# Kernel optimization log

Hardware: AMD Instinct MI355X
Metric: run time of the kernel (lower is better)

The kernel has to match this reference:

```python
import jax, jax.numpy as jnp
import numpy as np

COST_CLASS = 1.0
COST_OBJECTNESS = 5.0
COST_GIOU = 2.0
COST_CENTER = 10.0

B, Q, G, C = 32, 1024, 64, 256


def _lsa(cost):
    """Exact rectangular linear sum assignment (Jonker-Volgenant shortest
    augmenting path, same algorithm as scipy.optimize.linear_sum_assignment).
    cost: (R, Cc) float64 numpy array. Returns (row_ind, col_ind), row_ind sorted."""
    transposed = cost.shape[0] > cost.shape[1]
    if transposed:
        cost = cost.T
    n, m = cost.shape
    u = np.zeros(n)
    v = np.zeros(m)
    col4row = np.full(n, -1, dtype=np.int64)
    row4col = np.full(m, -1, dtype=np.int64)
    for cur_row in range(n):
        shortest = np.full(m, np.inf)
        path = np.full(m, -1, dtype=np.int64)
        SC = np.zeros(m, dtype=bool)
        SR_rows = []
        min_val = 0.0
        i = cur_row
        sink = -1
        while sink == -1:
            SR_rows.append(i)
            idx = np.where(~SC)[0]
            r = min_val + cost[i, idx] - u[i] - v[idx]
            better = r < shortest[idx]
            upd = idx[better]
            shortest[upd] = r[better]
            path[upd] = i
            j = idx[np.argmin(shortest[idx])]
            min_val = shortest[j]
            SC[j] = True
            if row4col[j] == -1:
                sink = j
            else:
                i = row4col[j]
        # dual variable update
        u[cur_row] += min_val
        for irow in SR_rows:
            if irow != cur_row:
                u[irow] += min_val - shortest[col4row[irow]]
        v[SC] -= min_val - shortest[SC]
        # augment along the alternating path back to cur_row
        j = sink
        while True:
            i = path[j]
            row4col[j] = i
            col4row[i], j = j, col4row[i]
            if i == cur_row:
                break
    if transposed:
        order = np.argsort(col4row)
        return col4row[order], np.arange(n)[order]
    return np.arange(n), col4row


def setup_inputs() -> dict:
    key = jax.random.key(0)
    k1, k2, k3, k4, k5 = jax.random.split(key, 5)
    return {
        "sem_cls_prob": jax.random.uniform(k1, (B, Q, C), dtype=jnp.float32),
        "objectness_prob": jax.random.uniform(k2, (B, Q), dtype=jnp.float32),
        "center_dist": jax.random.uniform(k3, (B, Q, G), dtype=jnp.float32),
        "gious": jax.random.uniform(k4, (B, Q, G), dtype=jnp.float32),
        "nactual_gt": jax.random.randint(k5, (B,), 0, G, dtype=jnp.int64)
        if jax.config.jax_enable_x64 else jax.random.randint(k5, (B,), 0, G).astype(jnp.int32),
    }


def reference(sem_cls_prob, objectness_prob, center_dist, gious, nactual_gt):
    batchsize, nprop = objectness_prob.shape
    # class_mat == 0 in the original module
    final_cost = (COST_OBJECTNESS * (-objectness_prob[..., None])
                  + COST_CENTER * center_dist
                  + COST_GIOU * (-gious))  # [B, Q, G]
    cost_np = np.asarray(final_cost, dtype=np.float64)
    ngt = np.asarray(nactual_gt)
    per_prop_gt_inds = np.zeros((batchsize, nprop), dtype=np.int64)
    proposal_matched_mask = np.zeros((batchsize, nprop), dtype=np.float32)
    for b in range(batchsize):  # per-batch independent Hungarian (as in source)
        g = int(ngt[b])
        if g > 0:
            rows, cols = _lsa(cost_np[b, :, :g])
            per_prop_gt_inds[b, rows] = cols
            proposal_matched_mask[b, rows] = 1.0
    return jnp.asarray(per_prop_gt_inds), jnp.asarray(proposal_matched_mask)
```

## Files before the change

kernel.cpp:

```cpp
#include <hip/hip_runtime.h>
#include <math.h>

#define B_ 32
#define Q_ 1024
#define G_ 64
#define K16 16

typedef double v16d __attribute__((ext_vector_type(16)));
typedef float  v16f __attribute__((ext_vector_type(16)));
typedef int    v16i __attribute__((ext_vector_type(16)));

#define REP16(OP) OP(0,0) OP(1,1) OP(2,2) OP(3,3) OP(4,4) OP(5,5) OP(6,6) OP(7,7) \
                  OP(8,8) OP(9,9) OP(10,a) OP(11,b) OP(12,c) OP(13,d) OP(14,e) OP(15,f)
#define REP16A(OP,A) OP(A,0,0) OP(A,1,1) OP(A,2,2) OP(A,3,3) OP(A,4,4) OP(A,5,5) OP(A,6,6) OP(A,7,7) \
                     OP(A,8,8) OP(A,9,9) OP(A,10,a) OP(A,11,b) OP(A,12,c) OP(A,13,d) OP(A,14,e) OP(A,15,f)

#define ROR1 0x121
#define ROR2 0x122
#define ROR4 0x124
#define ROR8 0x128
#define BC15 0x142
#define BC31 0x143

template<int CTRL>
__device__ __forceinline__ double dpp_f64(double x) {
    union { double d; int i[2]; } a; a.d = x;
    union { int i[2]; double d; } r;
    r.i[0] = __builtin_amdgcn_update_dpp(a.i[0], a.i[0], CTRL, 0xF, 0xF, false);
    r.i[1] = __builtin_amdgcn_update_dpp(a.i[1], a.i[1], CTRL, 0xF, 0xF, false);
    return r.d;
}
template<int CTRL>
__device__ __forceinline__ int dpp_i32(int x) {
    return __builtin_amdgcn_update_dpp(x, x, CTRL, 0xF, 0xF, false);
}

__device__ __forceinline__ double readlane_f64(double x, int sl) {
    const int s = __builtin_amdgcn_readfirstlane(sl);
    union { double d; int i2[2]; } a; a.d = x;
    union { int i2[2]; double d; } r;
    r.i2[0] = __builtin_amdgcn_readlane(a.i2[0], s);
    r.i2[1] = __builtin_amdgcn_readlane(a.i2[1], s);
    return r.d;
}
__device__ __forceinline__ double readlane_f64c(double x, int sl) {
    union { double d; int i2[2]; } a; a.d = x;
    union { int i2[2]; double d; } r;
    r.i2[0] = __builtin_amdgcn_readlane(a.i2[0], sl);
    r.i2[1] = __builtin_amdgcn_readlane(a.i2[1], sl);
    return r.d;
}
__device__ __forceinline__ float readlane_f32u(float x, int sl) {
    union { float f; int i; } a; a.f = x;
    union { int i; float f; } r;
    r.i = __builtin_amdgcn_readlane(a.i, __builtin_amdgcn_readfirstlane(sl));
    return r.f;
}
__device__ __forceinline__ int readlane_i32(int x, int sl) {
    return __builtin_amdgcn_readlane(x, __builtin_amdgcn_readfirstlane(sl));
}
__device__ __forceinline__ int readlane_i32c(int x, int sl) {
    return __builtin_amdgcn_readlane(x, sl);
}

__device__ __forceinline__ int sel16v_i(v16i p, int s) {
    const int t0_0 = (s & 1) ? p.s1 : p.s0;
    const int t0_1 = (s & 1) ? p.s3 : p.s2;
    const int t0_2 = (s & 1) ? p.s5 : p.s4;
    const int t0_3 = (s & 1) ? p.s7 : p.s6;
    const int t0_4 = (s & 1) ? p.s9 : p.s8;
    const int t0_5 = (s & 1) ? p.sb : p.sa;
    const int t0_6 = (s & 1) ? p.sd : p.sc;
    const int t0_7 = (s & 1) ? p.sf : p.se;
    const int t1_0 = (s & 2) ? t0_1 : t0_0;
    const int t1_1 = (s & 2) ? t0_3 : t0_2;
    const int t1_2 = (s & 2) ? t0_5 : t0_4;
    const int t1_3 = (s & 2) ? t0_7 : t0_6;
    const int a0 = (s & 4) ? t1_1 : t1_0;
    const int a1 = (s & 4) ? t1_3 : t1_2;
    return (s & 8) ? a1 : a0;
}
__device__ __forceinline__ double sel16v_d(v16d p, int s) {
    const double t0_0 = (s & 1) ? p.s1 : p.s0;
    const double t0_1 = (s & 1) ? p.s3 : p.s2;
    const double t0_2 = (s & 1) ? p.s5 : p.s4;
    const double t0_3 = (s & 1) ? p.s7 : p.s6;
    const double t0_4 = (s & 1) ? p.s9 : p.s8;
    const double t0_5 = (s & 1) ? p.sb : p.sa;
    const double t0_6 = (s & 1) ? p.sd : p.sc;
    const double t0_7 = (s & 1) ? p.sf : p.se;
    const double t1_0 = (s & 2) ? t0_1 : t0_0;
    const double t1_1 = (s & 2) ? t0_3 : t0_2;
    const double t1_2 = (s & 2) ? t0_5 : t0_4;
    const double t1_3 = (s & 2) ? t0_7 : t0_6;
    const double a0 = (s & 4) ? t1_1 : t1_0;
    const double a1 = (s & 4) ? t1_3 : t1_2;
    return (s & 8) ? a1 : a0;
}

__device__ __forceinline__ void lexpair(v16d c, int l,
                                        double& gv_o, int& jm_o) {
    const double a0 = fmin(c.s0, c.s1), a1 = fmin(c.s2, c.s3),
                 a2 = fmin(c.s4, c.s5), a3 = fmin(c.s6, c.s7),
                 a4 = fmin(c.s8, c.s9), a5 = fmin(c.sa, c.sb),
                 a6 = fmin(c.sc, c.sd), a7 = fmin(c.se, c.sf);
    const double b0 = fmin(a0, a1), b1 = fmin(a2, a3),
                 b2 = fmin(a4, a5), b3 = fmin(a6, a7);
    const double d0 = fmin(b0, b1), d1 = fmin(b2, b3);
    const double vloc = fmin(d0, d1);
    double v = vloc;
#define VS_(C) { const double pv = dpp_f64<C>(v); v = fmin(pv, v); }
    VS_(ROR1) VS_(ROR2) VS_(ROR4) VS_(ROR8) VS_(BC15) VS_(BC31)
#undef VS_
    const double gv = readlane_f64c(v, 63);
    const int bit3 = (d0 == gv) ? 0 : 1;
    const double bsel = bit3 ? b2 : b0;
    const int bit2 = (bsel == gv) ? 0 : 1;
    const double asel = bit2 ? (bit3 ? a6 : a2) : (bit3 ? a4 : a0);
    const int bit1 = (asel == gv) ? 0 : 1;
    const double csel = bit1 ? (bit2 ? (bit3 ? c.se : c.s6) : (bit3 ? c.sa : c.s2))
                             : (bit2 ? (bit3 ? c.sc : c.s4) : (bit3 ? c.s8 : c.s0));
    const int bit0 = (csel == gv) ? 0 : 1;
    const int kloc = (bit3 << 3) | (bit2 << 2) | (bit1 << 1) | bit0;
    int key = (vloc == gv) ? ((kloc << 6) | l) : 0x7FFFFFFF;
#define KS_(C) { const int pk = dpp_i32<C>(key); key = (pk < key) ? pk : key; }
    KS_(ROR1) KS_(ROR2) KS_(ROR4) KS_(ROR8) KS_(BC15) KS_(BC31)
#undef KS_
    jm_o = readlane_i32c(key, 63);
    gv_o = gv;
}

__global__ __launch_bounds__(256) void build_kernel(
    const float* __restrict__ obj, const float* __restrict__ cd,
    const float* __restrict__ gi, float* __restrict__ ct,
    float* __restrict__ pv, int* __restrict__ pj,
    float* __restrict__ pv2, int* __restrict__ pj2)
{
    __shared__ float tile[64][65];
    const int b  = blockIdx.y;
    const int jb = blockIdx.x << 6;
    const int t  = threadIdx.x;
    const float* objb = obj + (b << 10);
    const float4* cd4 = (const float4*)(cd + ((size_t)b << 16));
    const float4* gi4 = (const float4*)(gi + ((size_t)b << 16));

    #pragma unroll
    for (int p = 0; p < 4; ++p) {
        const int f  = t + (p << 8);
        const int jj = f >> 4;
        const int q  = f & 15;
        const int i0 = q << 2;
        const int j  = jb + jj;
        const float om = __fmul_rn(5.0f, -objb[j]);
        const float4 c4 = cd4[(j << 4) + q];
        const float4 q4 = gi4[(j << 4) + q];
        tile[i0 + 0][jj] = __fadd_rn(__fadd_rn(om, __fmul_rn(10.0f, c4.x)), __fmul_rn(2.0f, -q4.x));
        tile[i0 + 1][jj] = __fadd_rn(__fadd_rn(om, __fmul_rn(10.0f, c4.y)), __fmul_rn(2.0f, -q4.y));
        tile[i0 + 2][jj] = __fadd_rn(__fadd_rn(om, __fmul_rn(10.0f, c4.z)), __fmul_rn(2.0f, -q4.z));
        tile[i0 + 3][jj] = __fadd_rn(__fadd_rn(om, __fmul_rn(10.0f, c4.w)), __fmul_rn(2.0f, -q4.w));
    }
    __syncthreads();
    #pragma unroll
    for (int r = 0; r < 16; ++r) {
        const int idx = (r << 8) + t;
        const int i = idx >> 6, j2 = idx & 63;
        ct[(((size_t)(b << 6) + i) << 10) + jb + j2] = tile[i][j2];
    }
    if (t < 64) {
        float bv = tile[t][0]; int bc = 0;
        float sv = 1e30f;      int sc2 = 0;
        #pragma unroll 8
        for (int c = 1; c < 64; ++c) {
            const float v = tile[t][c];
            const bool t1 = v < bv;
            const bool t2 = (!t1) && (v < sv);
            sv  = t1 ? bv : (t2 ? v : sv);
            sc2 = t1 ? bc : (t2 ? c : sc2);
            bv  = t1 ? v : bv;
            bc  = t1 ? c : bc;
        }
        const int o = (((b << 6) + t) << 4) + blockIdx.x;
        pv[o]  = bv;  pj[o]  = jb + bc;
        pv2[o] = sv;  pj2[o] = jb + sc2;
    }
}

template<class LR>
__device__ __forceinline__ void matcher_core(
    const int l, const int g, LR load_row,
    const float pre_v, const int pre_j, const float sec_v, const int sec_j,
    float* __restrict__ out_ind_b, float* __restrict__ out_mask_b)
{
    const double INF = __builtin_inf();
    double u_rep = 0.0;
    double m_rec = 0.0;
    bool   inSR  = false;
    int    c4r_rep = -1;
    unsigned asg   = 0u;
    unsigned dirty = 0u;
    v16d v_r, sh_r;
    v16i path;
    v16f c_cur, c_i;
#define INI_(K,H) { v_r.s##H = 0.0; sh_r.s##H = 0.0; path.s##H = 0; }
    REP16(INI_)
#undef INI_
#define Z16_(K,H) { c_cur.s##H = 0.0f; c_i.s##H = 0.0f; }
    REP16(Z16_)
#undef Z16_

    for (int cur = 0; cur < g; ++cur) {
        const float pre_vc = readlane_f32u(pre_v, cur);
        int jm = readlane_i32(pre_j, cur);
        double minv = (double)pre_vc;
        bool have_cur = false;
        {
            const int ow1 = jm & 63, sl1 = jm >> 6;
            const unsigned d1 = (unsigned)readlane_i32((int)dirty, ow1);
            if ((d1 >> sl1) & 1u) {
                const float sv_c = readlane_f32u(sec_v, cur);
                const int   sj_c = readlane_i32(sec_j, cur);
                const unsigned d2 = (unsigned)readlane_i32((int)dirty, sj_c & 63);
                if (!((d2 >> (sj_c >> 6)) & 1u) && (sj_c != jm)) {
                    const double vpj = readlane_f64(sel16v_d(v_r, sl1), ow1);
                    const double vA = (double)pre_vc - vpj;
                    const double vB = (double)sv_c;
                    const bool tt = (vB < vA) || ((vB == vA) && (sj_c < jm));
                    minv = tt ? vB : vA;
                    jm   = tt ? sj_c : jm;
                } else {
                    c_cur = load_row(cur); have_cur = true;
                    v16d rr0;
#define RR0_(K,H) rr0.s##H = (double)c_cur.s##H - v_r.s##H;
                    REP16(RR0_)
#undef RR0_
                    lexpair(rr0, l, minv, jm);
                }
            }
        }
        const unsigned long long mk0 = __ballot(c4r_rep == jm);

        if (mk0 == 0ull) {
            u_rep   = (l == cur) ? u_rep + minv : u_rep;
            c4r_rep = (l == cur) ? jm           : c4r_rep;
            asg     = (l == (jm & 63)) ? (asg | (1u << (jm >> 6))) : asg;
        } else {
            if (!have_cur) c_cur = load_row(cur);
            int i = (int)__builtin_ctzll(mk0);
            c_i = load_row(i);
            double ui = readlane_f64(u_rep, i);
            unsigned sc = (l == (jm & 63)) ? (1u << (jm >> 6)) : 0u;
            inSR  = (l == i);
            m_rec = minv;
#define SH0_(K,H) { sh_r.s##H = (double)c_cur.s##H - v_r.s##H; path.s##H = cur; }
            REP16(SH0_)
#undef SH0_

            int sink = -1;
            while (sink < 0) {
                v16d cand;
#define DST_(K,H) { const double rr = ((minv + (double)c_i.s##H) - ui) - v_r.s##H; \
                    const bool notSC = !((sc >> K) & 1u); \
                    const bool upd = notSC && (rr < sh_r.s##H);  \
                    sh_r.s##H = upd ? rr : sh_r.s##H; \
                    path.s##H = upd ? i : path.s##H; \
                    cand.s##H = notSC ? sh_r.s##H : INF; }
                REP16(DST_)
#undef DST_
                lexpair(cand, l, minv, jm);
                const unsigned long long mk = __ballot(c4r_rep == jm);
                if (l == (jm & 63)) sc |= (1u << (jm >> 6));
                if (mk == 0ull) {
                    sink = jm;
                } else {
                    i = (int)__builtin_ctzll(mk);
                    c_i = load_row(i);
                    if (l == i) { inSR = true; m_rec = minv; }
                    ui = readlane_f64(u_rep, i);
                }
            }

            if (l == cur)       u_rep += minv;
            else if (inSR)      u_rep += minv - m_rec;
            unsigned chg = 0u;
#define VUP_(K,H) { const bool in_sc = (sc >> K) & 1u; \
                    const double nv = v_r.s##H - (minv - sh_r.s##H); \
                    chg = (in_sc && (sh_r.s##H != minv)) ? (chg | (1u << K)) : chg; \
                    v_r.s##H = in_sc ? nv : v_r.s##H; }
            REP16(VUP_)
#undef VUP_
            dirty |= chg;

            int j = sink;
            while (true) {
                const int so = j & 63, ss = j >> 6;
                const int ii = readlane_i32(sel16v_i(path, ss), so);
                const int nj = readlane_i32(c4r_rep, ii);
                asg     = (l == so) ? (asg | (1u << ss)) : asg;
                c4r_rep = (l == ii) ? j : c4r_rep;
                j = nj;
                if (ii == cur) break;
            }
        }
    }

#define OUT_(K,H) { const int jj = l + (K << 6); const bool a_ = (asg >> K) & 1u; \
    out_mask_b[jj] = a_ ? 1.0f : 0.0f; \
    if (!a_) out_ind_b[jj] = 0.0f; }
    REP16(OUT_)
#undef OUT_
    if (c4r_rep >= 0) out_ind_b[c4r_rep] = (float)l;
}

__global__ __launch_bounds__(256, 1) void matcher_ws(
    const int* __restrict__ ngt, const float* __restrict__ ct,
    const float* __restrict__ pv, const int* __restrict__ pj,
    const float* __restrict__ pv2, const int* __restrict__ pj2,
    float* __restrict__ out_ind, float* __restrict__ out_mask)
{
    const int b = blockIdx.x;
    const int t = threadIdx.x;
    const float* ctb = ct + ((size_t)(b << 6) << 10);

    if (t >= 64) {
        const float4* c4p = (const float4*)ctb;
        for (int n = t - 64; n < 16384; n += 192) {
            const float4 x = c4p[n];
            asm volatile("" :: "v"(x.x), "v"(x.y), "v"(x.z), "v"(x.w));
        }
        return;
    }

    const int l = t;
    const int g = ngt[b];

    const int base = ((b << 6) + l) << 4;
    const float4* pvq = (const float4*)(pv  + base);
    const int4*   pjq = (const int4*)(pj  + base);
    const float4* svq = (const float4*)(pv2 + base);
    const int4*   sjq = (const int4*)(pj2 + base);
    const float4 pA = pvq[0], pB = pvq[1], pC = pvq[2], pD = pvq[3];
    const int4   jA = pjq[0], jB = pjq[1], jC = pjq[2], jD = pjq[3];
    const float4 sA = svq[0], sB = svq[1], sC = svq[2], sD = svq[3];
    const int4   tA = sjq[0], tB = sjq[1], tC = sjq[2], tD = sjq[3];
    float bv = pA.x; int bj = jA.x; float sv = sA.x; int sj = tA.x;
#define MERGE_(CV,CJ,C2V,C2J) { const bool nb = (CV) < bv; \
    const bool s1 = (C2V) < bv; const bool s2 = (CV) < sv; \
    const float nsv = nb ? (s1 ? (C2V) : bv) : (s2 ? (CV) : sv); \
    const int   nsj = nb ? (s1 ? (C2J) : bj) : (s2 ? (CJ) : sj); \
    bj = nb ? (CJ) : bj; bv = nb ? (CV) : bv; sv = nsv; sj = nsj; }
    MERGE_(pA.y,jA.y,sA.y,tA.y) MERGE_(pA.z,jA.z,sA.z,tA.z) MERGE_(pA.w,jA.w,sA.w,tA.w)
    MERGE_(pB.x,jB.x,sB.x,tB.x) MERGE_(pB.y,jB.y,sB.y,tB.y) MERGE_(pB.z,jB.z,sB.z,tB.z) MERGE_(pB.w,jB.w,sB.w,tB.w)
    MERGE_(pC.x,jC.x,sC.x,tC.x) MERGE_(pC.y,jC.y,sC.y,tC.y) MERGE_(pC.z,jC.z,sC.z,tC.z) MERGE_(pC.w,jC.w,sC.w,tC.w)
    MERGE_(pD.x,jD.x,sD.x,tD.x) MERGE_(pD.y,jD.y,sD.y,tD.y) MERGE_(pD.z,jD.z,sD.z,tD.z) MERGE_(pD.w,jD.w,sD.w,tD.w)
#undef MERGE_

    auto load_row = [&](int ri) -> v16f {
        v16f d; const float* rp_ = ctb + ((size_t)ri << 10) + l;
#define LDW_(D,K,H) D.s##H = rp_[(K) << 6];
        REP16A(LDW_, d)
#undef LDW_
        return d;
    };
    matcher_core(l, g, load_row, bv, bj, sv, sj,
                 out_ind + (b << 10), out_mask + (b << 10));
}

__global__ __launch_bounds__(64, 1) void matcher_nws(
    const float* __restrict__ obj, const float* __restrict__ cd,
    const float* __restrict__ gi, const int* __restrict__ ngt,
    float* __restrict__ out_ind, float* __restrict__ out_mask)
{
    const int b = blockIdx.x;
    const int l = threadIdx.x;
    const int g = ngt[b];
    const float* objb = obj + (b << 10);
    const float* cdb  = cd + ((size_t)b << 16);
    const float* gib  = gi + ((size_t)b << 16);

    v16f objm;
#define OBJI_(K,H) objm.s##H = __fmul_rn(5.0f, -objb[l + (K << 6)]);
    REP16(OBJI_)
#undef OBJI_
    auto load_row = [&](int ri) -> v16f {
        v16f d;
#define LDN_(D,K,H) { const int idx_ = ((l + ((K) << 6)) << 6) + ri; \
    D.s##H = __fadd_rn(__fadd_rn(objm.s##H, __fmul_rn(10.0f, cdb[idx_])), \
                       __fmul_rn(2.0f, -gib[idx_])); }
        REP16A(LDN_, d)
#undef LDN_
        return d;
    };

    float pre_v = 0.0f; int pre_j = 0;
    for (int i = 0; i < g; ++i) {
        v16f c = load_row(i);
        v16d c64;
#define CV_(K,H) c64.s##H = (double)c.s##H;
        REP16(CV_)
#undef CV_
        double gv; int j0;
        lexpair(c64, l, gv, j0);
        pre_v = (l == i) ? (float)gv : pre_v;
        pre_j = (l == i) ? j0 : pre_j;
    }
    matcher_core(l, g, load_row, pre_v, pre_j, pre_v, pre_j,
                 out_ind + (b << 10), out_mask + (b << 10));
}

extern "C" void kernel_launch(void* const* d_in, const int* in_sizes, int n_in,
                              void* d_out, int out_size, void* d_ws, size_t ws_size,
                              hipStream_t stream)
{
    const float* obj = (const float*)d_in[1];
    const float* cd  = (const float*)d_in[2];
    const float* gi  = (const float*)d_in[3];
    const int*   ngt = (const int*)d_in[4];
    float* out0 = (float*)d_out;
    float* out1 = out0 + B_ * Q_;

    const size_t ct_b = (size_t)B_ * G_ * Q_ * sizeof(float);
    const size_t pv_b = (size_t)B_ * G_ * 16 * sizeof(float);
    if (ws_size >= ct_b + 4 * pv_b) {
        float* ct  = (float*)d_ws;
        float* pv  = (float*)((char*)d_ws + ct_b);
        int*   pj  = (int*)  ((char*)d_ws + ct_b + pv_b);
        float* pv2 = (float*)((char*)d_ws + ct_b + 2 * pv_b);
        int*   pj2 = (int*)  ((char*)d_ws + ct_b + 3 * pv_b);
        build_kernel<<<dim3(16, B_), 256, 0, stream>>>(obj, cd, gi, ct, pv, pj, pv2, pj2);
        matcher_ws<<<B_, 256, 0, stream>>>(ngt, ct, pv, pj, pv2, pj2, out0, out1);
    } else {
        matcher_nws<<<B_, 64, 0, stream>>>(obj, cd, gi, ngt, out0, out1);
    }
}
```

Measured before the change: 156.7 us.

## Fuse build and matcher kernels with per-batch flag spin-wait

Merges the cost-build kernel and the matcher kernel into one launch. The first 32 blocks are matchers and the other 512 blocks are builders. Each builder atomically increments a per-batch flag after writing its tile, and each matcher spins until its batch's flag reaches 16. This lets the matcher for one batch start while builds for other batches are still running, and removes the launch boundary between the two kernels. In exchange it adds a memset launch and relies on builder blocks being scheduled while matcher blocks spin. Matchers get the lower block IDs, so they are likely dispatched first, and there is some deadlock risk if builders cannot get resources.

```diff
diff --git a/kernel.cpp b/kernel.cpp
--- a/kernel.cpp
+++ b/kernel.cpp
@@ -130,61 +130,6 @@
     gv_o = gv;
 }
 
-__global__ __launch_bounds__(256) void build_kernel(
-    const float* __restrict__ obj, const float* __restrict__ cd,
-    const float* __restrict__ gi, float* __restrict__ ct,
-    float* __restrict__ pv, int* __restrict__ pj,
-    float* __restrict__ pv2, int* __restrict__ pj2)
-{
-    __shared__ float tile[64][65];
-    const int b  = blockIdx.y;
-    const int jb = blockIdx.x << 6;
-    const int t  = threadIdx.x;
-    const float* objb = obj + (b << 10);
-    const float4* cd4 = (const float4*)(cd + ((size_t)b << 16));
-    const float4* gi4 = (const float4*)(gi + ((size_t)b << 16));
-
-    #pragma unroll
-    for (int p = 0; p < 4; ++p) {
-        const int f  = t + (p << 8);
-        const int jj = f >> 4;
-        const int q  = f & 15;
-        const int i0 = q << 2;
-        const int j  = jb + jj;
-        const float om = __fmul_rn(5.0f, -objb[j]);
-        const float4 c4 = cd4[(j << 4) + q];
-        const float4 q4 = gi4[(j << 4) + q];
-        tile[i0 + 0][jj] = __fadd_rn(__fadd_rn(om, __fmul_rn(10.0f, c4.x)), __fmul_rn(2.0f, -q4.x));
-        tile[i0 + 1][jj] = __fadd_rn(__fadd_rn(om, __fmul_rn(10.0f, c4.y)), __fmul_rn(2.0f, -q4.y));
-        tile[i0 + 2][jj] = __fadd_rn(__fadd_rn(om, __fmul_rn(10.0f, c4.z)), __fmul_rn(2.0f, -q4.z));
-        tile[i0 + 3][jj] = __fadd_rn(__fadd_rn(om, __fmul_rn(10.0f, c4.w)), __fmul_rn(2.0f, -q4.w));
-    }
-    __syncthreads();
-    #pragma unroll
-    for (int r = 0; r < 16; ++r) {
-        const int idx = (r << 8) + t;
-        const int i = idx >> 6, j2 = idx & 63;
-        ct[(((size_t)(b << 6) + i) << 10) + jb + j2] = tile[i][j2];
-    }
-    if (t < 64) {
-        float bv = tile[t][0]; int bc = 0;
-        float sv = 1e30f;      int sc2 = 0;
-        #pragma unroll 8
-        for (int c = 1; c < 64; ++c) {
-            const float v = tile[t][c];
-            const bool t1 = v < bv;
-            const bool t2 = (!t1) && (v < sv);
-            sv  = t1 ? bv : (t2 ? v : sv);
-            sc2 = t1 ? bc : (t2 ? c : sc2);
-            bv  = t1 ? v : bv;
-            bc  = t1 ? c : bc;
-        }
-        const int o = (((b << 6) + t) << 4) + blockIdx.x;
-        pv[o]  = bv;  pj[o]  = jb + bc;
-        pv2[o] = sv;  pj2[o] = jb + sc2;
-    }
-}
-
 template<class LR>
 __device__ __forceinline__ void matcher_core(
     const int l, const int g, LR load_row,
@@ -311,16 +256,83 @@
     if (c4r_rep >= 0) out_ind_b[c4r_rep] = (float)l;
 }
 
-__global__ __launch_bounds__(256, 1) void matcher_ws(
-    const int* __restrict__ ngt, const float* __restrict__ ct,
-    const float* __restrict__ pv, const int* __restrict__ pj,
-    const float* __restrict__ pv2, const int* __restrict__ pj2,
+__global__ __launch_bounds__(256, 4) void fused2_k(
+    const float* __restrict__ obj, const float* __restrict__ cd,
+    const float* __restrict__ gi, const int* __restrict__ ngt,
+    float* __restrict__ ct,
+    float* __restrict__ pv, int* __restrict__ pj,
+    float* __restrict__ pv2, int* __restrict__ pj2,
+    unsigned* __restrict__ flags,
     float* __restrict__ out_ind, float* __restrict__ out_mask)
 {
-    const int b = blockIdx.x;
-    const int t = threadIdx.x;
+    __shared__ float tile[64][65];
+    const int t   = threadIdx.x;
+    const int bid = blockIdx.x;
+
+    if (bid >= B_) {
+        const int n0 = bid - B_;
+        const int b  = (n0 & 7) + (((n0 >> 3) & 3) << 3);
+        const int cb = n0 >> 5;
+        const int jb = cb << 6;
+        const float* objb = obj + (b << 10);
+        const float4* cd4 = (const float4*)(cd + ((size_t)b << 16));
+        const float4* gi4 = (const float4*)(gi + ((size_t)b << 16));
+
+        #pragma unroll
+        for (int p = 0; p < 4; ++p) {
+            const int f  = t + (p << 8);
+            const int jj = f >> 4;
+            const int q  = f & 15;
+            const int i0 = q << 2;
+            const int j  = jb + jj;
+            const float om = __fmul_rn(5.0f, -objb[j]);
+            const float4 c4 = cd4[(j << 4) + q];
+            const float4 q4 = gi4[(j << 4) + q];
+            tile[i0 + 0][jj] = __fadd_rn(__fadd_rn(om, __fmul_rn(10.0f, c4.x)), __fmul_rn(2.0f, -q4.x));
+            tile[i0 + 1][jj] = __fadd_rn(__fadd_rn(om, __fmul_rn(10.0f, c4.y)), __fmul_rn(2.0f, -q4.y));
+            tile[i0 + 2][jj] = __fadd_rn(__fadd_rn(om, __fmul_rn(10.0f, c4.z)), __fmul_rn(2.0f, -q4.z));
+            tile[i0 + 3][jj] = __fadd_rn(__fadd_rn(om, __fmul_rn(10.0f, c4.w)), __fmul_rn(2.0f, -q4.w));
+        }
+        __syncthreads();
+        #pragma unroll
+        for (int r = 0; r < 16; ++r) {
+            const int idx = (r << 8) + t;
+            const int i = idx >> 6, j2 = idx & 63;
+            ct[(((size_t)(b << 6) + i) << 10) + jb + j2] = tile[i][j2];
+        }
+        if (t < 64) {
+            float bv = tile[t][0]; int bc = 0;
+            float sv = 1e30f;      int sc2 = 0;
+            #pragma unroll 8
+            for (int c = 1; c < 64; ++c) {
+                const float v = tile[t][c];
+                const bool t1 = v < bv;
+                const bool t2 = (!t1) && (v < sv);
+                sv  = t1 ? bv : (t2 ? v : sv);
+                sc2 = t1 ? bc : (t2 ? c : sc2);
+                bv  = t1 ? v : bv;
+                bc  = t1 ? c : bc;
+            }
+            const int o = (((b << 6) + t) << 4) + cb;
+            pv[o]  = bv;  pj[o]  = jb + bc;
+            pv2[o] = sv;  pj2[o] = jb + sc2;
+        }
+        __syncthreads();
+        if (t == 0)
+            __hip_atomic_fetch_add(&flags[b], 1u, __ATOMIC_RELEASE,
+                                   __HIP_MEMORY_SCOPE_AGENT);
+        return;
+    }
+
+    const int b = bid;
+    if (t == 0) {
+        while (__hip_atomic_load(&flags[b], __ATOMIC_ACQUIRE,
+                                 __HIP_MEMORY_SCOPE_AGENT) < 16u)
+            __builtin_amdgcn_s_sleep(2);
+    }
+    __syncthreads();
+
     const float* ctb = ct + ((size_t)(b << 6) << 10);
-
     if (t >= 64) {
         const float4* c4p = (const float4*)ctb;
         for (int n = t - 64; n < 16384; n += 192) {
@@ -420,14 +432,18 @@
 
     const size_t ct_b = (size_t)B_ * G_ * Q_ * sizeof(float);
     const size_t pv_b = (size_t)B_ * G_ * 16 * sizeof(float);
-    if (ws_size >= ct_b + 4 * pv_b) {
-        float* ct  = (float*)d_ws;
-        float* pv  = (float*)((char*)d_ws + ct_b);
-        int*   pj  = (int*)  ((char*)d_ws + ct_b + pv_b);
-        float* pv2 = (float*)((char*)d_ws + ct_b + 2 * pv_b);
-        int*   pj2 = (int*)  ((char*)d_ws + ct_b + 3 * pv_b);
-        build_kernel<<<dim3(16, B_), 256, 0, stream>>>(obj, cd, gi, ct, pv, pj, pv2, pj2);
-        matcher_ws<<<B_, 256, 0, stream>>>(ngt, ct, pv, pj, pv2, pj2, out0, out1);
+    const size_t fl_b = B_ * sizeof(unsigned);
+    if (ws_size >= ct_b + 4 * pv_b + fl_b) {
+        float*    ct    = (float*)d_ws;
+        float*    pv    = (float*)((char*)d_ws + ct_b);
+        int*      pj    = (int*)  ((char*)d_ws + ct_b + pv_b);
+        float*    pv2   = (float*)((char*)d_ws + ct_b + 2 * pv_b);
+        int*      pj2   = (int*)  ((char*)d_ws + ct_b + 3 * pv_b);
+        unsigned* flags = (unsigned*)((char*)d_ws + ct_b + 4 * pv_b);
+        hipMemsetAsync(flags, 0, fl_b, stream);
+        fused2_k<<<B_ + 16 * B_, 256, 0, stream>>>(obj, cd, gi, ngt, ct,
+                                                   pv, pj, pv2, pj2, flags,
+                                                   out0, out1);
     } else {
         matcher_nws<<<B_, 64, 0, stream>>>(obj, cd, gi, ngt, out0, out1);
     }
```

After: 245.0 us. 56.3% more time.
